# Optimization experiments

Measured on AMD Instinct MI355X. Metric: run time of the kernel, lower is better.

Reference implementation:

```python
import jax, jax.numpy as jnp
import numpy as np

TEMPERATURE = 0.05
EPS = 1e-6
N, D = 8192, 64


def setup_inputs() -> dict:
    key = jax.random.key(0)
    k1, k2 = jax.random.split(key)
    anchor_embeddings = jax.random.normal(k1, (N, D), dtype=jnp.float32)
    positive_embeddings = jax.random.normal(k2, (N, D), dtype=jnp.float32)
    return {"anchor_embeddings": anchor_embeddings,
            "positive_embeddings": positive_embeddings}


def _cos_matrix(x, y, nx, ny):
    # pairwise cosine sim with torch CosineSimilarity eps semantics:
    # dot / max(||x||*||y||, eps)
    return (x @ y.T) / jnp.maximum(nx[:, None] * ny[None, :], EPS)


def reference(anchor_embeddings, positive_embeddings):
    a, p = anchor_embeddings, positive_embeddings
    na = jnp.linalg.norm(a, axis=-1)  # [N]
    npn = jnp.linalg.norm(p, axis=-1)  # [N]

    inv_t = 1.0 / TEMPERATURE
    S_ap = _cos_matrix(a, p, na, npn)  # [N, N]
    S_aa = _cos_matrix(a, a, na, na)   # [N, N]
    S_pp = _cos_matrix(p, p, npn, npn)  # [N, N]

    E_ap = jnp.exp(S_ap * inv_t)
    E_aa = jnp.exp(S_aa * inv_t)
    E_pp = jnp.exp(S_pp * inv_t)

    self_term = jnp.exp(jnp.asarray(inv_t, dtype=a.dtype))  # exp(1/T)
    # partition_i = sum_j E_ap[i,j] + sum_j E_aa[i,j] - e^{1/T}
    #             + sum_j E_ap[j,i] + sum_j E_pp[j,i] - e^{1/T}
    partition = (E_ap.sum(axis=1) + E_aa.sum(axis=1)
                 + E_ap.sum(axis=0) + E_pp.sum(axis=0)
                 - 2.0 * self_term)

    # loss = -mean_i log( exp(cos(a_i,p_i)/T) / partition_i )
    pos_logit = jnp.diagonal(S_ap) * inv_t
    loss = -jnp.mean(pos_logit - jnp.log(partition))
    return loss
```

## Files before the change

kernel.cpp:

```cpp
#include <hip/hip_runtime.h>
#include <hip/hip_bf16.h>
#include <math.h>

#define N 8192
#define D 64
#define INVT 20.0f
#define EPS 1e-6f
#define ZSCALE 5.3715835f

typedef __attribute__((ext_vector_type(8))) short bf16x8;
typedef __attribute__((ext_vector_type(4))) float f32x4;

#if __has_builtin(__builtin_amdgcn_exp2f)
#define EXP2F(x) __builtin_amdgcn_exp2f(x)
#else
#define EXP2F(x) exp2f(x)
#endif


__device__ __forceinline__ void unrank(int t, int& bi, int& bj) {
    int b = (int)((257.0f - sqrtf(66049.0f - 8.0f * (float)t)) * 0.5f);
    while (b * (257 - b) / 2 > t) --b;
    while ((b + 1) * (256 - b) / 2 <= t) ++b;
    bi = b;
    bj = b + (t - b * (257 - b) / 2);
}

__global__ __launch_bounds__(256) void prep_kernel(
    const float* __restrict__ A, const float* __restrict__ P,
    __hip_bfloat16* __restrict__ Zn, float* __restrict__ diag20,
    float* __restrict__ part, float* __restrict__ lacc, unsigned* __restrict__ cnt) {
    if (blockIdx.x < 64) part[blockIdx.x * 256 + threadIdx.x] = 0.0f;
    else if (blockIdx.x == 64 && threadIdx.x == 0) { *lacc = 0.0f; *cnt = 0u; }

    const int lane = threadIdx.x & 63;
    const int w    = threadIdx.x >> 6;
    const int r    = blockIdx.x * 4 + w;
    const int u    = lane >> 3, sub = lane & 7;
    const int upos = (u >> 2) * 64 + (u & 3) * 16;

    float a = A[r * D + lane];
    float p = P[r * D + lane];
    float sa = a * a, sp = p * p, dp = a * p;
    #pragma unroll
    for (int off = 1; off < 64; off <<= 1) {
        sa += __shfl_xor(sa, off, 64);
        sp += __shfl_xor(sp, off, 64);
        dp += __shfl_xor(dp, off, 64);
    }
    float na  = sqrtf(sa);
    float npn = sqrtf(sp);
    {
        int g = r >> 4, l2 = r & 15;
        Zn[(g * 128 + upos + l2) * 8 + sub] = __float2bfloat16(a * (ZSCALE / na));
    }
    {
        int R = N + r; int g = R >> 4, l2 = R & 15;
        Zn[(g * 128 + upos + l2) * 8 + sub] = __float2bfloat16(p * (ZSCALE / npn));
    }
    if (lane == 0)
        diag20[r] = (dp / fmaxf(na * npn, EPS)) * INVT;
}

__global__ __launch_bounds__(256, 4) void tiles_kernel(
    const __hip_bfloat16* __restrict__ Zn, float* __restrict__ part) {
    __shared__ float rs[4][16][68];
    __shared__ float merged[2][128];

    const int tid = threadIdx.x;
    const int lane = tid & 63, w = tid >> 6;
    const int wr = w >> 1, wc = w & 1;
    const int ln = lane & 15, q = lane >> 4;
    const bf16x8* Zf = (const bf16x8*)Zn;
    const f32x4 zero = {0.0f, 0.0f, 0.0f, 0.0f};

    const int b = (int)blockIdx.x;
    const int ntiles = (b < 64) ? 9 : 8;
    int bi, bj;
    unrank(b * 8 + ((b < 64) ? b : 64), bi, bj);

    bf16x8 af[4][2];
    #pragma unroll
    for (int ii = 0; ii < 4; ++ii) {
        int ga = bi * 8 + wr * 4 + ii;
        af[ii][0] = Zf[ga * 128 + lane];
        af[ii][1] = Zf[ga * 128 + 64 + lane];
    }

    float rsum[4][4] = {{0.0f}};

    for (int t = 0; t < ntiles; ++t) {
        bf16x8 bv[4][2];
        #pragma unroll
        for (int ii = 0; ii < 4; ++ii) {
            int gb = bj * 8 + wc * 4 + ii;
            bv[ii][0] = Zf[gb * 128 + lane];
            bv[ii][1] = Zf[gb * 128 + 64 + lane];
        }

        const bool dwave = (bi == bj) && (wr == wc);
        float csum[4] = {0.0f, 0.0f, 0.0f, 0.0f};
        #pragma unroll
        for (int ii = 0; ii < 4; ++ii) {
            f32x4 acc[4];
            #pragma unroll
            for (int jj = 0; jj < 4; ++jj)
                acc[jj] = __builtin_amdgcn_mfma_f32_16x16x32_bf16(
                    af[ii][0], bv[jj][0], zero, 0, 0, 0);
            #pragma unroll
            for (int jj = 0; jj < 4; ++jj)
                acc[jj] = __builtin_amdgcn_mfma_f32_16x16x32_bf16(
                    af[ii][1], bv[jj][1], acc[jj], 0, 0, 0);

            #pragma unroll
            for (int jj = 0; jj < 4; ++jj) {
                f32x4 e;
                #pragma unroll
                for (int r = 0; r < 4; ++r) e[r] = EXP2F(acc[jj][r]);
                if (dwave && (ii == jj)) {
                    #pragma unroll
                    for (int r = 0; r < 4; ++r)
                        if (ln == q * 4 + r) e[r] = 0.0f;
                }
                #pragma unroll
                for (int r = 0; r < 4; ++r) rsum[ii][r] += e[r];
                csum[jj] += (e[0] + e[1]) + (e[2] + e[3]);
            }
        }

        if (bi != bj) {
            float cs0 = csum[0], cs1 = csum[1], cs2 = csum[2], cs3 = csum[3];
            cs0 += __shfl_xor(cs0, 16, 64); cs0 += __shfl_xor(cs0, 32, 64);
            cs1 += __shfl_xor(cs1, 16, 64); cs1 += __shfl_xor(cs1, 32, 64);
            cs2 += __shfl_xor(cs2, 16, 64); cs2 += __shfl_xor(cs2, 32, 64);
            cs3 += __shfl_xor(cs3, 16, 64); cs3 += __shfl_xor(cs3, 32, 64);
            float cval = (q == 0) ? cs0 : (q == 1) ? cs1 : (q == 2) ? cs2 : cs3;
            atomicAdd(part + bj * 128 + wc * 64 + lane, cval);
        }

        if (t + 1 < ntiles) {
            if (bj == 127) {
                #pragma unroll
                for (int ii = 0; ii < 4; ++ii)
                    *(f32x4*)&rs[w][ln][ii * 16 + q * 4] = *(const f32x4*)&rsum[ii][0];
                float rowsum = 0.0f;
                #pragma unroll
                for (int l = 0; l < 16; ++l) rowsum += rs[w][l][lane];
                merged[wc][wr * 64 + lane] = rowsum;
                __syncthreads();
                if (tid < 128)
                    atomicAdd(part + bi * 128 + tid, merged[0][tid] + merged[1][tid]);
                __syncthreads();
                #pragma unroll
                for (int ii = 0; ii < 4; ++ii) {
                    #pragma unroll
                    for (int r = 0; r < 4; ++r) rsum[ii][r] = 0.0f;
                }
                ++bi; bj = bi;
                #pragma unroll
                for (int ii = 0; ii < 4; ++ii) {
                    int ga = bi * 8 + wr * 4 + ii;
                    af[ii][0] = Zf[ga * 128 + lane];
                    af[ii][1] = Zf[ga * 128 + 64 + lane];
                }
            } else {
                ++bj;
            }
        }
    }

    #pragma unroll
    for (int ii = 0; ii < 4; ++ii)
        *(f32x4*)&rs[w][ln][ii * 16 + q * 4] = *(const f32x4*)&rsum[ii][0];
    float rowsum = 0.0f;
    #pragma unroll
    for (int l = 0; l < 16; ++l) rowsum += rs[w][l][lane];
    merged[wc][wr * 64 + lane] = rowsum;
    __syncthreads();
    if (tid < 128)
        atomicAdd(part + bi * 128 + tid, merged[0][tid] + merged[1][tid]);
}

__global__ __launch_bounds__(256) void loss_kernel(
    const float* __restrict__ part, const float* __restrict__ diag20,
    float* __restrict__ lacc, unsigned* __restrict__ cnt, float* __restrict__ out) {
    int i = blockIdx.x * 256 + threadIdx.x;
    float v = logf(part[i] + part[N + i]) - diag20[i];
    #pragma unroll
    for (int off = 32; off > 0; off >>= 1) v += __shfl_down(v, off, 64);
    __shared__ float wsm[4];
    int lane = threadIdx.x & 63, wv = threadIdx.x >> 6;
    if (lane == 0) wsm[wv] = v;
    __syncthreads();
    if (threadIdx.x == 0) {
        atomicAdd(lacc, wsm[0] + wsm[1] + wsm[2] + wsm[3]);
        __threadfence();
        unsigned old = atomicAdd(cnt, 1u);
        if (old == (N / 256 - 1)) {
            float tot = atomicAdd(lacc, 0.0f);
            out[0] = tot * (1.0f / (float)N);
        }
    }
}

extern "C" void kernel_launch(void* const* d_in, const int* in_sizes, int n_in,
                              void* d_out, int out_size, void* d_ws, size_t ws_size,
                              hipStream_t stream) {
    const float* A = (const float*)d_in[0];
    const float* P = (const float*)d_in[1];

    __hip_bfloat16* Zn = (__hip_bfloat16*)d_ws;
    float* diag20 = (float*)((char*)d_ws + 2u * N * D * sizeof(__hip_bfloat16));
    float* part   = diag20 + N;
    float* lacc   = part + 2 * N;
    unsigned* cnt = (unsigned*)(lacc + 1);

    prep_kernel<<<N / 4, 256, 0, stream>>>(A, P, Zn, diag20, part, lacc, cnt);

    tiles_kernel<<<1024, 256, 0, stream>>>(Zn, part);

    loss_kernel<<<N / 256, 256, 0, stream>>>(part, diag20, lacc, cnt, (float*)d_out);
}
```

Before: 112.7 us.

## Prefetch next B tile in registers and split work into 4-tile blocks

The tile loop is unrolled into four fixed tiles per block. The B-fragment loads for the next tile are issued right after each column group's MFMAs, so global loads overlap with the exp and reduction work. The MFMA issue order is switched to column-major, and the grid grows from 1024 to 2064 blocks of exactly 4 tiles each, which removes the 9-versus-8 imbalance and adds more parallelism. The cost is more per-block fixed overhead, more row-flush atomics, and higher register pressure from keeping the prefetched fragments live.

```diff
diff --git a/kernel.cpp b/kernel.cpp
--- a/kernel.cpp
+++ b/kernel.cpp
@@ -62,6 +62,134 @@
         diag20[r] = (dp / fmaxf(na * npn, EPS)) * INVT;
 }
 
+
+#define ROW_FLUSH()                                                            \
+    {                                                                          \
+        *(f32x4*)&rs[w][ln][0 * 16 + q * 4] = rsum0;                           \
+        *(f32x4*)&rs[w][ln][1 * 16 + q * 4] = rsum1;                           \
+        *(f32x4*)&rs[w][ln][2 * 16 + q * 4] = rsum2;                           \
+        *(f32x4*)&rs[w][ln][3 * 16 + q * 4] = rsum3;                           \
+        float rowsum = 0.0f;                                                   \
+        _Pragma("unroll")                                                      \
+        for (int l = 0; l < 16; ++l) rowsum += rs[w][l][lane];                 \
+        merged[wc][wr * 64 + lane] = rowsum;                                   \
+        __syncthreads();                                                       \
+        if (tid < 128)                                                         \
+            atomicAdd(part + bi * 128 + tid, merged[0][tid] + merged[1][tid]); \
+    }
+
+#define TILE_T(HAVE_NEXT)                                                      \
+    {                                                                          \
+        const bool dwave = (bi == bj) && (wr == wc);                           \
+        const int nbi = (bj == 127) ? (bi + 1) : bi;                           \
+        const int nbj = (bj == 127) ? (bi + 1) : (bj + 1);                     \
+        float csum0 = 0.0f, csum1 = 0.0f, csum2 = 0.0f, csum3 = 0.0f;          \
+        _Pragma("unroll")                                                      \
+        for (int jj = 0; jj < 4; ++jj) {                                       \
+            f32x4 acc0 = __builtin_amdgcn_mfma_f32_16x16x32_bf16(              \
+                af[0][0], bv[jj][0], zero, 0, 0, 0);                           \
+            f32x4 acc1 = __builtin_amdgcn_mfma_f32_16x16x32_bf16(              \
+                af[1][0], bv[jj][0], zero, 0, 0, 0);                           \
+            f32x4 acc2 = __builtin_amdgcn_mfma_f32_16x16x32_bf16(              \
+                af[2][0], bv[jj][0], zero, 0, 0, 0);                           \
+            f32x4 acc3 = __builtin_amdgcn_mfma_f32_16x16x32_bf16(              \
+                af[3][0], bv[jj][0], zero, 0, 0, 0);                           \
+            acc0 = __builtin_amdgcn_mfma_f32_16x16x32_bf16(                    \
+                af[0][1], bv[jj][1], acc0, 0, 0, 0);                           \
+            acc1 = __builtin_amdgcn_mfma_f32_16x16x32_bf16(                    \
+                af[1][1], bv[jj][1], acc1, 0, 0, 0);                           \
+            acc2 = __builtin_amdgcn_mfma_f32_16x16x32_bf16(                    \
+                af[2][1], bv[jj][1], acc2, 0, 0, 0);                           \
+            acc3 = __builtin_amdgcn_mfma_f32_16x16x32_bf16(                    \
+                af[3][1], bv[jj][1], acc3, 0, 0, 0);                           \
+                     \
+            if (HAVE_NEXT) {                                                   \
+                int gb = nbj * 8 + wc * 4 + jj;                                \
+                bv[jj][0] = Zf[gb * 128 + lane];                               \
+                bv[jj][1] = Zf[gb * 128 + 64 + lane];                          \
+            }                                                                  \
+            float cst = 0.0f;                                                  \
+            {                                                                  \
+                f32x4 e;                                                       \
+                _Pragma("unroll")                                              \
+                for (int r = 0; r < 4; ++r) e[r] = EXP2F(acc0[r]);             \
+                if (dwave && jj == 0) {                                        \
+                    _Pragma("unroll")                                          \
+                    for (int r = 0; r < 4; ++r)                                \
+                        if (ln == q * 4 + r) e[r] = 0.0f;                      \
+                }                                                              \
+                rsum0 += e; cst += (e[0] + e[1]) + (e[2] + e[3]);              \
+            }                                                                  \
+            {                                                                  \
+                f32x4 e;                                                       \
+                _Pragma("unroll")                                              \
+                for (int r = 0; r < 4; ++r) e[r] = EXP2F(acc1[r]);             \
+                if (dwave && jj == 1) {                                        \
+                    _Pragma("unroll")                                          \
+                    for (int r = 0; r < 4; ++r)                                \
+                        if (ln == q * 4 + r) e[r] = 0.0f;                      \
+                }                                                              \
+                rsum1 += e; cst += (e[0] + e[1]) + (e[2] + e[3]);              \
+            }                                                                  \
+            {                                                                  \
+                f32x4 e;                                                       \
+                _Pragma("unroll")                                              \
+                for (int r = 0; r < 4; ++r) e[r] = EXP2F(acc2[r]);             \
+                if (dwave && jj == 2) {                                        \
+                    _Pragma("unroll")                                          \
+                    for (int r = 0; r < 4; ++r)                                \
+                        if (ln == q * 4 + r) e[r] = 0.0f;                      \
+                }                                                              \
+                rsum2 += e; cst += (e[0] + e[1]) + (e[2] + e[3]);              \
+            }                                                                  \
+            {                                                                  \
+                f32x4 e;                                                       \
+                _Pragma("unroll")                                              \
+                for (int r = 0; r < 4; ++r) e[r] = EXP2F(acc3[r]);             \
+                if (dwave && jj == 3) {                                        \
+                    _Pragma("unroll")                                          \
+                    for (int r = 0; r < 4; ++r)                                \
+                        if (ln == q * 4 + r) e[r] = 0.0f;                      \
+                }                                                              \
+                rsum3 += e; cst += (e[0] + e[1]) + (e[2] + e[3]);              \
+            }                                                                  \
+            if (jj == 0) csum0 = cst;                                          \
+            else if (jj == 1) csum1 = cst;                                     \
+            else if (jj == 2) csum2 = cst;                                     \
+            else csum3 = cst;                                                  \
+        }                                                                      \
+            \
+        if (bi != bj) {                                                        \
+            csum0 += __shfl_xor(csum0, 16, 64);                                \
+            csum0 += __shfl_xor(csum0, 32, 64);                                \
+            csum1 += __shfl_xor(csum1, 16, 64);                                \
+            csum1 += __shfl_xor(csum1, 32, 64);                                \
+            csum2 += __shfl_xor(csum2, 16, 64);                                \
+            csum2 += __shfl_xor(csum2, 32, 64);                                \
+            csum3 += __shfl_xor(csum3, 16, 64);                                \
+            csum3 += __shfl_xor(csum3, 32, 64);                                \
+            float cval = (q == 0) ? csum0 : (q == 1) ? csum1                   \
+                       : (q == 2) ? csum2 : csum3;                             \
+            atomicAdd(part + bj * 128 + wc * 64 + lane, cval);                 \
+        }                                                                      \
+        if (HAVE_NEXT) {                                                       \
+            if (bj == 127) {                                                   \
+                ROW_FLUSH();                                                   \
+                __syncthreads();                                               \
+                rsum0 = zero; rsum1 = zero; rsum2 = zero; rsum3 = zero;        \
+                bi = nbi; bj = nbj;                                            \
+                _Pragma("unroll")                                              \
+                for (int ii = 0; ii < 4; ++ii) {                               \
+                    int ga = bi * 8 + wr * 4 + ii;                             \
+                    af[ii][0] = Zf[ga * 128 + lane];                           \
+                    af[ii][1] = Zf[ga * 128 + 64 + lane];                      \
+                }                                                              \
+            } else {                                                           \
+                bi = nbi; bj = nbj;                                            \
+            }                                                                  \
+        }                                                                      \
+    }
+
 __global__ __launch_bounds__(256, 4) void tiles_kernel(
     const __hip_bfloat16* __restrict__ Zn, float* __restrict__ part) {
     __shared__ float rs[4][16][68];
@@ -74,10 +202,8 @@
     const bf16x8* Zf = (const bf16x8*)Zn;
     const f32x4 zero = {0.0f, 0.0f, 0.0f, 0.0f};
 
-    const int b = (int)blockIdx.x;
-    const int ntiles = (b < 64) ? 9 : 8;
     int bi, bj;
-    unrank(b * 8 + ((b < 64) ? b : 64), bi, bj);
+    unrank((int)blockIdx.x * 4, bi, bj);
 
     bf16x8 af[4][2];
     #pragma unroll
@@ -86,99 +212,22 @@
         af[ii][0] = Zf[ga * 128 + lane];
         af[ii][1] = Zf[ga * 128 + 64 + lane];
     }
-
-    float rsum[4][4] = {{0.0f}};
-
-    for (int t = 0; t < ntiles; ++t) {
-        bf16x8 bv[4][2];
-        #pragma unroll
-        for (int ii = 0; ii < 4; ++ii) {
-            int gb = bj * 8 + wc * 4 + ii;
-            bv[ii][0] = Zf[gb * 128 + lane];
-            bv[ii][1] = Zf[gb * 128 + 64 + lane];
-        }
-
-        const bool dwave = (bi == bj) && (wr == wc);
-        float csum[4] = {0.0f, 0.0f, 0.0f, 0.0f};
-        #pragma unroll
-        for (int ii = 0; ii < 4; ++ii) {
-            f32x4 acc[4];
-            #pragma unroll
-            for (int jj = 0; jj < 4; ++jj)
-                acc[jj] = __builtin_amdgcn_mfma_f32_16x16x32_bf16(
-                    af[ii][0], bv[jj][0], zero, 0, 0, 0);
-            #pragma unroll
-            for (int jj = 0; jj < 4; ++jj)
-                acc[jj] = __builtin_amdgcn_mfma_f32_16x16x32_bf16(
-                    af[ii][1], bv[jj][1], acc[jj], 0, 0, 0);
-
-            #pragma unroll
-            for (int jj = 0; jj < 4; ++jj) {
-                f32x4 e;
-                #pragma unroll
-                for (int r = 0; r < 4; ++r) e[r] = EXP2F(acc[jj][r]);
-                if (dwave && (ii == jj)) {
-                    #pragma unroll
-                    for (int r = 0; r < 4; ++r)
-                        if (ln == q * 4 + r) e[r] = 0.0f;
-                }
-                #pragma unroll
-                for (int r = 0; r < 4; ++r) rsum[ii][r] += e[r];
-                csum[jj] += (e[0] + e[1]) + (e[2] + e[3]);
-            }
-        }
-
-        if (bi != bj) {
-            float cs0 = csum[0], cs1 = csum[1], cs2 = csum[2], cs3 = csum[3];
-            cs0 += __shfl_xor(cs0, 16, 64); cs0 += __shfl_xor(cs0, 32, 64);
-            cs1 += __shfl_xor(cs1, 16, 64); cs1 += __shfl_xor(cs1, 32, 64);
-            cs2 += __shfl_xor(cs2, 16, 64); cs2 += __shfl_xor(cs2, 32, 64);
-            cs3 += __shfl_xor(cs3, 16, 64); cs3 += __shfl_xor(cs3, 32, 64);
-            float cval = (q == 0) ? cs0 : (q == 1) ? cs1 : (q == 2) ? cs2 : cs3;
-            atomicAdd(part + bj * 128 + wc * 64 + lane, cval);
-        }
-
-        if (t + 1 < ntiles) {
-            if (bj == 127) {
-                #pragma unroll
-                for (int ii = 0; ii < 4; ++ii)
-                    *(f32x4*)&rs[w][ln][ii * 16 + q * 4] = *(const f32x4*)&rsum[ii][0];
-                float rowsum = 0.0f;
-                #pragma unroll
-                for (int l = 0; l < 16; ++l) rowsum += rs[w][l][lane];
-                merged[wc][wr * 64 + lane] = rowsum;
-                __syncthreads();
-                if (tid < 128)
-                    atomicAdd(part + bi * 128 + tid, merged[0][tid] + merged[1][tid]);
-                __syncthreads();
-                #pragma unroll
-                for (int ii = 0; ii < 4; ++ii) {
-                    #pragma unroll
-                    for (int r = 0; r < 4; ++r) rsum[ii][r] = 0.0f;
-                }
-                ++bi; bj = bi;
-                #pragma unroll
-                for (int ii = 0; ii < 4; ++ii) {
-                    int ga = bi * 8 + wr * 4 + ii;
-                    af[ii][0] = Zf[ga * 128 + lane];
-                    af[ii][1] = Zf[ga * 128 + 64 + lane];
-                }
-            } else {
-                ++bj;
-            }
-        }
-    }
-
-    #pragma unroll
-    for (int ii = 0; ii < 4; ++ii)
-        *(f32x4*)&rs[w][ln][ii * 16 + q * 4] = *(const f32x4*)&rsum[ii][0];
-    float rowsum = 0.0f;
-    #pragma unroll
-    for (int l = 0; l < 16; ++l) rowsum += rs[w][l][lane];
-    merged[wc][wr * 64 + lane] = rowsum;
-    __syncthreads();
-    if (tid < 128)
-        atomicAdd(part + bi * 128 + tid, merged[0][tid] + merged[1][tid]);
+    bf16x8 bv[4][2];
+    #pragma unroll
+    for (int jj = 0; jj < 4; ++jj) {
+        int gb = bj * 8 + wc * 4 + jj;
+        bv[jj][0] = Zf[gb * 128 + lane];
+        bv[jj][1] = Zf[gb * 128 + 64 + lane];
+    }
+
+    f32x4 rsum0 = zero, rsum1 = zero, rsum2 = zero, rsum3 = zero;
+
+    TILE_T(true)
+    TILE_T(true)
+    TILE_T(true)
+    TILE_T(false)
+
+    ROW_FLUSH();
 }
 
 __global__ __launch_bounds__(256) void loss_kernel(
@@ -217,7 +266,7 @@
 
     prep_kernel<<<N / 4, 256, 0, stream>>>(A, P, Zn, diag20, part, lacc, cnt);
 
-    tiles_kernel<<<1024, 256, 0, stream>>>(Zn, part);
+    tiles_kernel<<<2064, 256, 0, stream>>>(Zn, part);
 
     loss_kernel<<<N / 256, 256, 0, stream>>>(part, diag20, lacc, cnt, (float*)d_out);
 }
```

Result: slower. 150.2 us (+33.3%).
